# Kernel tuning notes

Measured on AMD Instinct MI355X. Metric: run time of the kernel, lower is better.

## Reference

```python
import jax, jax.numpy as jnp
import numpy as np

D_MODEL = 1024
NUM_HEADS = 16
HEAD_DIM = D_MODEL // NUM_HEADS


def setup_inputs() -> dict:
    key = jax.random.key(0)
    k_x, k_wqkv, k_bqkv, k_wout, k_bout = jax.random.split(key, 5)
    B, S = 2, 2048
    x = jax.random.normal(k_x, (B, S, D_MODEL), dtype=jnp.float32)
    # haiku Linear: y = x @ W + b, W shape [in, out]
    init_scale = 1.0 / np.sqrt(D_MODEL)
    W_qkv = jax.random.normal(k_wqkv, (D_MODEL, 3 * D_MODEL), dtype=jnp.float32) * init_scale
    b_qkv = jnp.zeros((3 * D_MODEL,), dtype=jnp.float32)
    W_out = jax.random.normal(k_wout, (D_MODEL, D_MODEL), dtype=jnp.float32) * init_scale
    b_out = jnp.zeros((D_MODEL,), dtype=jnp.float32)
    return {"x": x, "W_qkv": W_qkv, "b_qkv": b_qkv, "W_out": W_out, "b_out": b_out}


def reference(x, W_qkv, b_qkv, W_out, b_out):
    B, S, _ = x.shape
    qkv = x @ W_qkv + b_qkv                      # [B, S, 3*D]
    q, k, v = jnp.split(qkv, 3, axis=-1)         # each [B, S, D]
    # [B, S, D] -> [B, H, S, Hd]
    def heads(t):
        return t.reshape(B, S, NUM_HEADS, HEAD_DIM).transpose(0, 2, 1, 3)
    q, k, v = heads(q), heads(k), heads(v)
    scale = jnp.sqrt(jnp.float32(HEAD_DIM)).astype(x.dtype)
    attn = jnp.einsum('bhqd,bhkd->bhqk', q, k) / scale   # [B, H, S, S]
    attn = jax.nn.softmax(attn, axis=-1)
    out = jnp.einsum('bhqk,bhkd->bhqd', attn, v)          # [B, H, S, Hd]
    out = out.transpose(0, 2, 1, 3).reshape(B, S, D_MODEL)
    return out @ W_out + b_out
```

## Files before the change

kernel.cpp:

```cpp
#include <hip/hip_runtime.h>
#include <stdint.h>


#define BATCH 2
#define SEQ 2048
#define DM 1024
#define NH 16
#define HD 64
#define M_TOT 4096
#define QSCALE 0.18033688011112042f

typedef __bf16 bf16x8 __attribute__((ext_vector_type(8)));
typedef __bf16 bf16x4 __attribute__((ext_vector_type(4)));
typedef float  f32x4  __attribute__((ext_vector_type(4)));

__device__ __forceinline__ void gld_lds16(const void* g, void* l) {
    __builtin_amdgcn_global_load_lds(
        (const __attribute__((address_space(1))) uint32_t*)g,
        (__attribute__((address_space(3))) uint32_t*)l, 16, 0, 0);
}

__launch_bounds__(256)
__global__ void prep_kernel(const float* __restrict__ x,
                            const float* __restrict__ Wqkv,
                            const float* __restrict__ Wout,
                            __bf16* __restrict__ xs,
                            __bf16* __restrict__ wqt,
                            __bf16* __restrict__ wot)
{
    __shared__ float T[64][69];
    const int tid = threadIdx.x;
    const int blk = blockIdx.x;

    if (blk < 4096) {
        const int i  = blk * 256 + tid;
        const int m  = i >> 8;
        const int c4 = (i & 255) * 4;
        float4 v = *reinterpret_cast<const float4*>(&x[(size_t)m * DM + c4]);
        float a[4] = {v.x, v.y, v.z, v.w};
        bf16x4 hi, lo;
        #pragma unroll
        for (int j = 0; j < 4; ++j) {
            __bf16 h = (__bf16)a[j];
            hi[j] = h;
            lo[j] = (__bf16)(a[j] - (float)h);
        }
        *reinterpret_cast<bf16x4*>(&xs[(size_t)m * (2*DM) + c4]) = hi;
        *reinterpret_cast<bf16x4*>(&xs[(size_t)m * (2*DM) + DM + c4]) = lo;
        return;
    }

    const int bb = (blk < 4864) ? blk - 4096 : blk - 4864;
    const float* W = (blk < 4864) ? Wqkv : Wout;
    __bf16* Wt     = (blk < 4864) ? wqt  : wot;
    const int N    = (blk < 4864) ? 3 * DM : DM;
    const int k0 = (bb & 15) * 64, n0 = (bb >> 4) * 64;

    {
        const int kr = tid >> 4, c4 = (tid & 15) * 4;
        #pragma unroll
        for (int i = 0; i < 4; ++i) {
            float4 v = *reinterpret_cast<const float4*>(
                &W[(size_t)(k0 + kr + 16 * i) * N + n0 + c4]);
            *reinterpret_cast<float4*>(&T[kr + 16 * i][c4]) = v;
        }
    }
    __syncthreads();
    {
        const int n = tid >> 2, kc = (tid & 3) * 16;
        __bf16 hi[16], lo[16];
        #pragma unroll
        for (int j = 0; j < 16; ++j) {
            float v = T[kc + j][n];
            __bf16 h = (__bf16)v;
            hi[j] = h;
            lo[j] = (__bf16)(v - (float)h);
        }
        const size_t ro = (size_t)(n0 + n) * (2*DM) + k0 + kc;
        *reinterpret_cast<bf16x8*>(&Wt[ro])          = *reinterpret_cast<bf16x8*>(&hi[0]);
        *reinterpret_cast<bf16x8*>(&Wt[ro + 8])      = *reinterpret_cast<bf16x8*>(&hi[8]);
        *reinterpret_cast<bf16x8*>(&Wt[ro + DM])     = *reinterpret_cast<bf16x8*>(&lo[0]);
        *reinterpret_cast<bf16x8*>(&Wt[ro + DM + 8]) = *reinterpret_cast<bf16x8*>(&lo[8]);
    }
}

__launch_bounds__(512, 2)
__global__ void gemm_qkv_kernel(const __bf16* __restrict__ A,
                                const __bf16* __restrict__ Bt,
                                const float* __restrict__ bias,
                                __bf16* __restrict__ qs,
                                __bf16* __restrict__ khi_g,
                                __bf16* __restrict__ klo_g,
                                __bf16* __restrict__ vt_g)
{
    __shared__ __align__(16) __bf16 pool[65536];

    const int tid  = threadIdx.x;
    const int w    = tid >> 6;
    const int lane = tid & 63;
    const int n16  = lane & 15;
    const int quad = lane >> 4;

    const int wg = (blockIdx.x & 7) * 24 + (blockIdx.x >> 3);
    const int bm = (wg & 15) * 256;
    const int bn = (wg >> 4) * 256;

    const int wm = (w >> 2) * 128;
    const int wn = (w & 3) * 64;

    const int r0 = tid >> 3;
    const int c0 = ((tid & 7) ^ (r0 & 7));

    auto stage = [&](int p, int kcol, int nbuf) {
        __bf16* dst = pool + nbuf * 32768 + p * 8192;
        const __bf16* gsrc = (p < 2)
            ? A  + (size_t)(bm + p * 128) * (2*DM) + kcol
            : Bt + (size_t)(bn + (p - 2) * 128) * (2*DM) + kcol;
        gld_lds16(gsrc + (size_t)r0 * (2*DM) + c0 * 8,        dst + (size_t)tid * 8);
        gld_lds16(gsrc + (size_t)(r0 + 64) * (2*DM) + c0 * 8, dst + (size_t)(512 + tid) * 8);
    };

    const int rowA = (wm + n16) * 64;
    const int rowB = (wn + n16) * 64;
    const int sx0 = ((quad)     ^ (n16 & 7)) << 3;
    const int sx1 = ((4 + quad) ^ (n16 & 7)) << 3;

    f32x4 acc[8][4] = {};
    bf16x8 af[4][2], bf0[2][2], bf1[2][2];

    stage(0, 0, 0); stage(1, 0, 0); stage(2, 0, 0); stage(3, 0, 0);

    #pragma unroll 2
    for (int t = 0; t < 48; ++t) {
        const int buf = t & 1;
        const __bf16* bufA = pool + buf * 32768;
        const __bf16* bufB = bufA + 16384;
        const int nbuf = buf ^ 1;
        const bool pre = (t < 47);
        const int tt = t + 1;
        const int a_k = (tt < 16) ? tt * 64 : tt * 64 - DM;
        const int b_k = (tt < 32) ? tt * 64 : tt * 64 - 2 * DM;

        if (pre) {
            stage(0, a_k, nbuf);
            asm volatile("s_waitcnt vmcnt(2)" ::: "memory");
        } else {
            asm volatile("s_waitcnt vmcnt(0)" ::: "memory");
        }
        __builtin_amdgcn_s_barrier();
        __builtin_amdgcn_sched_barrier(0);
        #pragma unroll
        for (int i = 0; i < 4; ++i) {
            af[i][0] = *reinterpret_cast<const bf16x8*>(bufA + rowA + i * 1024 + sx0);
            af[i][1] = *reinterpret_cast<const bf16x8*>(bufA + rowA + i * 1024 + sx1);
        }
        #pragma unroll
        for (int j = 0; j < 2; ++j) {
            bf0[j][0] = *reinterpret_cast<const bf16x8*>(bufB + rowB + j * 1024 + sx0);
            bf0[j][1] = *reinterpret_cast<const bf16x8*>(bufB + rowB + j * 1024 + sx1);
        }
        asm volatile("s_waitcnt lgkmcnt(0)" ::: "memory");
        __builtin_amdgcn_sched_barrier(0);
        __builtin_amdgcn_s_setprio(1);
        #pragma unroll
        for (int i = 0; i < 4; ++i)
            #pragma unroll
            for (int j = 0; j < 2; ++j) {
                acc[i][j] = __builtin_amdgcn_mfma_f32_16x16x32_bf16(af[i][0], bf0[j][0], acc[i][j], 0, 0, 0);
                acc[i][j] = __builtin_amdgcn_mfma_f32_16x16x32_bf16(af[i][1], bf0[j][1], acc[i][j], 0, 0, 0);
            }
        __builtin_amdgcn_s_setprio(0);

        #pragma unroll
        for (int j = 0; j < 2; ++j) {
            bf1[j][0] = *reinterpret_cast<const bf16x8*>(bufB + rowB + (2 + j) * 1024 + sx0);
            bf1[j][1] = *reinterpret_cast<const bf16x8*>(bufB + rowB + (2 + j) * 1024 + sx1);
        }
        if (pre) stage(1, a_k, nbuf);
        __builtin_amdgcn_s_barrier();
        __builtin_amdgcn_sched_barrier(0);
        asm volatile("s_waitcnt lgkmcnt(0)" ::: "memory");
        __builtin_amdgcn_sched_barrier(0);
        __builtin_amdgcn_s_setprio(1);
        #pragma unroll
        for (int i = 0; i < 4; ++i)
            #pragma unroll
            for (int j = 0; j < 2; ++j) {
                acc[i][2 + j] = __builtin_amdgcn_mfma_f32_16x16x32_bf16(af[i][0], bf1[j][0], acc[i][2 + j], 0, 0, 0);
                acc[i][2 + j] = __builtin_amdgcn_mfma_f32_16x16x32_bf16(af[i][1], bf1[j][1], acc[i][2 + j], 0, 0, 0);
            }
        __builtin_amdgcn_s_setprio(0);

        #pragma unroll
        for (int i = 0; i < 4; ++i) {
            af[i][0] = *reinterpret_cast<const bf16x8*>(bufA + rowA + (4 + i) * 1024 + sx0);
            af[i][1] = *reinterpret_cast<const bf16x8*>(bufA + rowA + (4 + i) * 1024 + sx1);
        }
        if (pre) stage(2, b_k, nbuf);
        __builtin_amdgcn_s_barrier();
        __builtin_amdgcn_sched_barrier(0);
        asm volatile("s_waitcnt lgkmcnt(0)" ::: "memory");
        __builtin_amdgcn_sched_barrier(0);
        __builtin_amdgcn_s_setprio(1);
        #pragma unroll
        for (int i = 0; i < 4; ++i)
            #pragma unroll
            for (int j = 0; j < 2; ++j) {
                acc[4 + i][j] = __builtin_amdgcn_mfma_f32_16x16x32_bf16(af[i][0], bf0[j][0], acc[4 + i][j], 0, 0, 0);
                acc[4 + i][j] = __builtin_amdgcn_mfma_f32_16x16x32_bf16(af[i][1], bf0[j][1], acc[4 + i][j], 0, 0, 0);
            }
        __builtin_amdgcn_s_setprio(0);

        if (pre) stage(3, b_k, nbuf);
        __builtin_amdgcn_s_barrier();
        __builtin_amdgcn_sched_barrier(0);
        __builtin_amdgcn_s_setprio(1);
        #pragma unroll
        for (int i = 0; i < 4; ++i)
            #pragma unroll
            for (int j = 0; j < 2; ++j) {
                acc[4 + i][2 + j] = __builtin_amdgcn_mfma_f32_16x16x32_bf16(af[i][0], bf1[j][0], acc[4 + i][2 + j], 0, 0, 0);
                acc[4 + i][2 + j] = __builtin_amdgcn_mfma_f32_16x16x32_bf16(af[i][1], bf1[j][1], acc[4 + i][2 + j], 0, 0, 0);
            }
        __builtin_amdgcn_s_setprio(0);
    }

    __syncthreads();

    const int colb = bn + wn;
    const int part = colb >> 10;
    const int hh   = (colb & 1023) >> 6;

    float bv[4];
    #pragma unroll
    for (int j = 0; j < 4; ++j) bv[j] = bias[colb + j * 16 + n16];

    __bf16* scrH = pool + w * 4608;
    __bf16* scrL = scrH + 2304;
    const int lr = lane & 31, hc = lane >> 5;

    #pragma unroll
    for (int mi = 0; mi < 2; ++mi) {
        const int brow = bm + wm + mi * 64;
        const int b    = brow >> 11;
        const int s0   = brow & 2047;
        const int bh   = b * NH + hh;
        const int kt   = s0 >> 6;
        const size_t tb = ((size_t)bh * 32 + kt) * 4096;

        #pragma unroll
        for (int p = 0; p < 2; ++p) {
            if (part == 2) {
                #pragma unroll
                for (int jj = 0; jj < 2; ++jj) {
                    const int j = 2 * p + jj;
                    #pragma unroll
                    for (int i = 0; i < 4; ++i) {
                        bf16x4 v4;
                        #pragma unroll
                        for (int r = 0; r < 4; ++r)
                            v4[r] = (__bf16)(acc[4 * mi + i][j][r] + bv[j]);
                        *reinterpret_cast<bf16x4*>(
                            &scrH[(jj * 16 + n16) * 72 + i * 16 + quad * 4]) = v4;
                    }
                }
            } else {
                #pragma unroll
                for (int ii = 0; ii < 2; ++ii) {
                    const int i = 2 * p + ii;
                    #pragma unroll
                    for (int j = 0; j < 4; ++j) {
                        #pragma unroll
                        for (int r = 0; r < 4; ++r) {
                            float val = acc[4 * mi + i][j][r] + bv[j];
                            if (part == 0) val *= QSCALE;
                            __bf16 h = (__bf16)val;
                            const int so = (ii * 16 + quad * 4 + r) * 72 + j * 16 + n16;
                            scrH[so] = h;
                            scrL[so] = (__bf16)(val - (float)h);
                        }
                    }
                }
            }
            __syncthreads();

            if (part == 0) {
                const size_t qbase = ((size_t)bh * SEQ + s0 + 32 * p + lr) * 128;
                #pragma unroll
                for (int t = 0; t < 4; ++t) {
                    const int ch = hc * 4 + t;
                    *reinterpret_cast<bf16x8*>(&qs[qbase + ch * 8]) =
                        *reinterpret_cast<const bf16x8*>(&scrH[lr * 72 + ch * 8]);
                    *reinterpret_cast<bf16x8*>(&qs[qbase + 64 + ch * 8]) =
                        *reinterpret_cast<const bf16x8*>(&scrL[lr * 72 + ch * 8]);
                }
            } else if (part == 1) {
                const int kr = 32 * p + lr;
                #pragma unroll
                for (int t = 0; t < 4; ++t) {
                    const int ch = hc * 4 + t;
                    const int src = (ch ^ (lr & 7)) * 8;
                    *reinterpret_cast<bf16x8*>(&khi_g[tb + kr * 64 + ch * 8]) =
                        *reinterpret_cast<const bf16x8*>(&scrH[lr * 72 + src]);
                    *reinterpret_cast<bf16x8*>(&klo_g[tb + kr * 64 + ch * 8]) =
                        *reinterpret_cast<const bf16x8*>(&scrL[lr * 72 + src]);
                }
            } else {
                const int d = 32 * p + lr;
                #pragma unroll
                for (int t = 0; t < 4; ++t) {
                    const int ch = hc * 4 + t;
                    const int src = (ch ^ (lr & 7)) * 8;
                    *reinterpret_cast<bf16x8*>(&vt_g[tb + d * 64 + ch * 8]) =
                        *reinterpret_cast<const bf16x8*>(&scrH[lr * 72 + src]);
                }
            }
            __syncthreads();
        }
    }
}

__launch_bounds__(256)
__global__ void gemm_out_kernel(const __bf16* __restrict__ A,
                                const __bf16* __restrict__ Bt,
                                const float* __restrict__ bias,
                                float* __restrict__ out)
{
    __shared__ __align__(16) __bf16 AsH[128 * 32];
    __shared__ __align__(16) __bf16 AsL[128 * 32];
    __shared__ __align__(16) __bf16 BsH[64 * 32];
    __shared__ __align__(16) __bf16 BsL[64 * 32];

    const int tid  = threadIdx.x;
    const int w    = tid >> 6;
    const int lane = tid & 63;
    const int n16  = lane & 15;
    const int quad = lane >> 4;
    const int bm = blockIdx.x * 128, bn = blockIdx.y * 64;
    const int wm = (w & 1) * 64,     wn = (w >> 1) * 32;

    const int srow = tid >> 2, sc = (tid & 3) * 8;
    const __bf16* Ar = A  + (size_t)(bm + srow) * (2*DM) + sc;
    const __bf16* Br = Bt + (size_t)(bn + srow) * (2*DM) + sc;

    f32x4 acc[4][2] = {};

    for (int k0 = 0; k0 < DM; k0 += 32) {
        __syncthreads();
        gld_lds16(Ar + k0,                         &AsH[(size_t)tid * 8]);
        gld_lds16(Ar + k0 + (size_t)64*2*DM,       &AsH[(size_t)(256 + tid) * 8]);
        gld_lds16(Ar + DM + k0,                    &AsL[(size_t)tid * 8]);
        gld_lds16(Ar + DM + k0 + (size_t)64*2*DM,  &AsL[(size_t)(256 + tid) * 8]);
        gld_lds16(Br + k0,                         &BsH[(size_t)tid * 8]);
        gld_lds16(Br + DM + k0,                    &BsL[(size_t)tid * 8]);
        __syncthreads();

        bf16x8 afh[4], afl[4], bfh[2], bfl[2];
        #pragma unroll
        for (int i = 0; i < 4; ++i) {
            const int ro = (wm + i*16 + n16) * 32 + quad * 8;
            afh[i] = *reinterpret_cast<const bf16x8*>(&AsH[ro]);
            afl[i] = *reinterpret_cast<const bf16x8*>(&AsL[ro]);
        }
        #pragma unroll
        for (int j = 0; j < 2; ++j) {
            const int ro = (wn + j*16 + n16) * 32 + quad * 8;
            bfh[j] = *reinterpret_cast<const bf16x8*>(&BsH[ro]);
            bfl[j] = *reinterpret_cast<const bf16x8*>(&BsL[ro]);
        }
        #pragma unroll
        for (int i = 0; i < 4; ++i)
            #pragma unroll
            for (int j = 0; j < 2; ++j) {
                acc[i][j] = __builtin_amdgcn_mfma_f32_16x16x32_bf16(afh[i], bfh[j], acc[i][j], 0, 0, 0);
                acc[i][j] = __builtin_amdgcn_mfma_f32_16x16x32_bf16(afh[i], bfl[j], acc[i][j], 0, 0, 0);
                acc[i][j] = __builtin_amdgcn_mfma_f32_16x16x32_bf16(afl[i], bfh[j], acc[i][j], 0, 0, 0);
            }
    }

    #pragma unroll
    for (int j = 0; j < 2; ++j) {
        const int col = bn + wn + j * 16 + n16;
        const float bvv = bias[col];
        #pragma unroll
        for (int i = 0; i < 4; ++i) {
            const int row0 = bm + wm + i * 16 + quad * 4;
            #pragma unroll
            for (int r = 0; r < 4; ++r)
                out[(size_t)(row0 + r) * DM + col] = acc[i][j][r] + bvv;
        }
    }
}

__launch_bounds__(256, 2)
__global__ void flash_attn_v5_kernel(const __bf16* __restrict__ qs,
                                     const __bf16* __restrict__ khi_g,
                                     const __bf16* __restrict__ klo_g,
                                     const __bf16* __restrict__ vt_g,
                                     __bf16* __restrict__ ctx2)
{
    __shared__ __align__(16) __bf16 Khi[2][4096];
    __shared__ __align__(16) __bf16 Klo[2][4096];
    __shared__ __align__(16) __bf16 Vt [2][4096];
    __shared__ __align__(16) __bf16 Ps [8192];

    const int tid  = threadIdx.x;
    const int w    = tid >> 6;
    const int lane = tid & 63;
    const int n16  = lane & 15;
    const int quad = lane >> 4;
    const int bid  = blockIdx.x;
    const int bh = (bid & 7) * 4 + (bid >> 7);
    const int qt = (bid >> 3) & 15;

    bf16x8 qh[2][2], ql[2][2];
    #pragma unroll
    for (int qg = 0; qg < 2; ++qg) {
        const size_t qrow =
            ((size_t)bh * SEQ + qt * 128 + w * 32 + qg * 16 + n16) * 128;
        #pragma unroll
        for (int s2 = 0; s2 < 2; ++s2) {
            qh[qg][s2] = *reinterpret_cast<const bf16x8*>(&qs[qrow + s2 * 32 + quad * 8]);
            ql[qg][s2] = *reinterpret_cast<const bf16x8*>(&qs[qrow + 64 + s2 * 32 + quad * 8]);
        }
    }

    f32x4 o[2][4] = {};
    float l_lane[2] = {};

    for (int kt2 = 0; kt2 < 16; ++kt2) {
        __syncthreads();
        {
            const int buf = w >> 1;
            const size_t tb = ((size_t)bh * 32 + kt2 * 2 + buf) * 4096;
            #pragma unroll
            for (int t = 0; t < 12; ++t) {
                const int rem = (w & 1) * 12 + t;
                const int arr = rem >> 3, sub = rem & 7;
                const int eo = sub * 512 + lane * 8;
                const __bf16* g = (arr == 0 ? khi_g : arr == 1 ? klo_g : vt_g) + tb + eo;
                __bf16* l = (arr == 0 ? Khi[buf] : arr == 1 ? Klo[buf] : Vt[buf]) + eo;
                gld_lds16(g, l);
            }
        }
        __syncthreads();

        #pragma unroll
        for (int hf = 0; hf < 2; ++hf) {
            const __bf16* KhiB = Khi[hf];
            const __bf16* KloB = Klo[hf];
            const __bf16* VtB  = Vt[hf];

            #pragma unroll
            for (int kg = 0; kg < 4; ++kg) {
                const int r = kg * 16 + n16;
                const int o0 = r * 64 + ((quad ^ (r & 7)) << 3);
                const int o1 = r * 64 + (((4 + quad) ^ (r & 7)) << 3);
                bf16x8 kh0 = *reinterpret_cast<const bf16x8*>(&KhiB[o0]);
                bf16x8 kl0 = *reinterpret_cast<const bf16x8*>(&KloB[o0]);
                bf16x8 kh1 = *reinterpret_cast<const bf16x8*>(&KhiB[o1]);
                bf16x8 kl1 = *reinterpret_cast<const bf16x8*>(&KloB[o1]);
                #pragma unroll
                for (int qg = 0; qg < 2; ++qg) {
                    f32x4 sa = {}, sb = {};
                    sa = __builtin_amdgcn_mfma_f32_16x16x32_bf16(kh0, qh[qg][0], sa, 0, 0, 0);
                    sb = __builtin_amdgcn_mfma_f32_16x16x32_bf16(kh1, qh[qg][1], sb, 0, 0, 0);
                    sa = __builtin_amdgcn_mfma_f32_16x16x32_bf16(kl0, qh[qg][0], sa, 0, 0, 0);
                    sb = __builtin_amdgcn_mfma_f32_16x16x32_bf16(kl1, qh[qg][1], sb, 0, 0, 0);
                    sa = __builtin_amdgcn_mfma_f32_16x16x32_bf16(kh0, ql[qg][0], sa, 0, 0, 0);
                    sb = __builtin_amdgcn_mfma_f32_16x16x32_bf16(kh1, ql[qg][1], sb, 0, 0, 0);
                    f32x4 st = sa + sb;

                    f32x4 pp;
                    #pragma unroll
                    for (int r2 = 0; r2 < 4; ++r2) pp[r2] = exp2f(st[r2]);
                    l_lane[qg] += (pp[0] + pp[1]) + (pp[2] + pp[3]);

                    bf16x4 p4;
                    #pragma unroll
                    for (int r2 = 0; r2 < 4; ++r2) p4[r2] = (__bf16)pp[r2];
                    const int prow = w * 32 + qg * 16 + n16;
                    const int ch2 = kg * 2 + (quad >> 1);
                    const int off = prow * 64 + ((ch2 ^ (prow & 7)) << 3) + (quad & 1) * 4;
                    *reinterpret_cast<bf16x4*>(&Ps[off]) = p4;
                }
            }

            bf16x8 pa[2][2];
            #pragma unroll
            for (int qg = 0; qg < 2; ++qg) {
                const int prow = w * 32 + qg * 16 + n16;
                #pragma unroll
                for (int s2 = 0; s2 < 2; ++s2)
                    pa[qg][s2] = *reinterpret_cast<const bf16x8*>(
                        &Ps[prow * 64 + (((s2 * 4 + quad) ^ (prow & 7)) << 3)]);
            }
            #pragma unroll
            for (int c = 0; c < 4; ++c) {
                const int vr = c * 16 + n16;
                bf16x8 vb0 = *reinterpret_cast<const bf16x8*>(
                    &VtB[vr * 64 + ((quad ^ (vr & 7)) << 3)]);
                bf16x8 vb1 = *reinterpret_cast<const bf16x8*>(
                    &VtB[vr * 64 + (((4 + quad) ^ (vr & 7)) << 3)]);
                #pragma unroll
                for (int qg = 0; qg < 2; ++qg) {
                    o[qg][c] = __builtin_amdgcn_mfma_f32_16x16x32_bf16(pa[qg][0], vb0, o[qg][c], 0, 0, 0);
                    o[qg][c] = __builtin_amdgcn_mfma_f32_16x16x32_bf16(pa[qg][1], vb1, o[qg][c], 0, 0, 0);
                }
            }
        }
    }

    #pragma unroll
    for (int qg = 0; qg < 2; ++qg) {
        l_lane[qg] += __shfl_xor(l_lane[qg], 16, 64);
        l_lane[qg] += __shfl_xor(l_lane[qg], 32, 64);
    }

    const int b = bh >> 4, hh = bh & 15;
    #pragma unroll
    for (int qg = 0; qg < 2; ++qg) {
        #pragma unroll
        for (int r2 = 0; r2 < 4; ++r2) {
            const float l = __shfl(l_lane[qg], (quad << 4) + quad * 4 + r2, 64);
            const float linv = 1.0f / l;
            const int srow = qt * 128 + w * 32 + qg * 16 + quad * 4 + r2;
            const size_t rowoff = (size_t)(b * SEQ + srow) * (2*DM);
            #pragma unroll
            for (int c = 0; c < 4; ++c) {
                const int col = hh * HD + c * 16 + n16;
                float v = o[qg][c][r2] * linv;
                __bf16 h = (__bf16)v;
                ctx2[rowoff + col] = h;
                ctx2[rowoff + DM + col] = (__bf16)(v - (float)h);
            }
        }
    }
}

extern "C" void kernel_launch(void* const* d_in, const int* in_sizes, int n_in,
                              void* d_out, int out_size, void* d_ws, size_t ws_size,
                              hipStream_t stream)
{
    const float* x    = (const float*)d_in[0];
    const float* Wqkv = (const float*)d_in[1];
    const float* bqkv = (const float*)d_in[2];
    const float* Wout = (const float*)d_in[3];
    const float* bout = (const float*)d_in[4];
    float* out = (float*)d_out;

    char* ws = (char*)d_ws;
    __bf16* xs   = (__bf16*)(ws);
    __bf16* ctx2 = xs;
    __bf16* wqt  = (__bf16*)(ws + (size_t)16 * 1024 * 1024);
    __bf16* wot  = (__bf16*)(ws + (size_t)28 * 1024 * 1024);
    __bf16* qsb  = (__bf16*)(ws + (size_t)32 * 1024 * 1024);
    __bf16* khi  = (__bf16*)(ws + (size_t)48 * 1024 * 1024);
    __bf16* klo  = (__bf16*)(ws + (size_t)56 * 1024 * 1024);
    __bf16* vt   = (__bf16*)(ws + (size_t)64 * 1024 * 1024);

    prep_kernel<<<dim3(5120), 256, 0, stream>>>(x, Wqkv, Wout, xs, wqt, wot);
    gemm_qkv_kernel<<<dim3(192), 512, 0, stream>>>(
        xs, wqt, bqkv, qsb, khi, klo, vt);
    flash_attn_v5_kernel<<<dim3(512), 256, 0, stream>>>(qsb, khi, klo, vt, ctx2);
    gemm_out_kernel<<<dim3(M_TOT / 128, DM / 64), 256, 0, stream>>>(
        ctx2, wot, bout, out);
}
```

Baseline: 284.0 us.

## Double-buffer attention K/V tiles and issue all GEMM prefetches up front

In the QKV GEMM main loop, all four global-to-LDS stage copies for the next k-tile are now issued at the start of the iteration instead of being spread between the MFMA phases. The wait becomes vmcnt(8) so only the current tile's loads must land. In the attention kernel, the old loop loaded two 64-key half tiles into LDS with two block-wide syncs and then computed on them. It is replaced by a 32-step double-buffered pipeline: the next tile is prefetched asynchronously while the current one is computed, with a trailing barrier guarding buffer reuse. The aim is to hide global load latency behind MFMA work, at the cost of more in-flight loads and a few extra barriers.

```diff
diff --git a/kernel.cpp b/kernel.cpp
--- a/kernel.cpp
+++ b/kernel.cpp
@@ -143,7 +143,10 @@
 
         if (pre) {
             stage(0, a_k, nbuf);
-            asm volatile("s_waitcnt vmcnt(2)" ::: "memory");
+            stage(1, a_k, nbuf);
+            stage(2, b_k, nbuf);
+            stage(3, b_k, nbuf);
+            asm volatile("s_waitcnt vmcnt(8)" ::: "memory");
         } else {
             asm volatile("s_waitcnt vmcnt(0)" ::: "memory");
         }
@@ -176,7 +179,6 @@
             bf1[j][0] = *reinterpret_cast<const bf16x8*>(bufB + rowB + (2 + j) * 1024 + sx0);
             bf1[j][1] = *reinterpret_cast<const bf16x8*>(bufB + rowB + (2 + j) * 1024 + sx1);
         }
-        if (pre) stage(1, a_k, nbuf);
         __builtin_amdgcn_s_barrier();
         __builtin_amdgcn_sched_barrier(0);
         asm volatile("s_waitcnt lgkmcnt(0)" ::: "memory");
@@ -196,7 +198,6 @@
             af[i][0] = *reinterpret_cast<const bf16x8*>(bufA + rowA + (4 + i) * 1024 + sx0);
             af[i][1] = *reinterpret_cast<const bf16x8*>(bufA + rowA + (4 + i) * 1024 + sx1);
         }
-        if (pre) stage(2, b_k, nbuf);
         __builtin_amdgcn_s_barrier();
         __builtin_amdgcn_sched_barrier(0);
         asm volatile("s_waitcnt lgkmcnt(0)" ::: "memory");
@@ -211,7 +212,6 @@
             }
         __builtin_amdgcn_s_setprio(0);
 
-        if (pre) stage(3, b_k, nbuf);
         __builtin_amdgcn_s_barrier();
         __builtin_amdgcn_sched_barrier(0);
         __builtin_amdgcn_s_setprio(1);
@@ -428,87 +428,97 @@
     f32x4 o[2][4] = {};
     float l_lane[2] = {};
 
-    for (int kt2 = 0; kt2 < 16; ++kt2) {
-        __syncthreads();
-        {
-            const int buf = w >> 1;
-            const size_t tb = ((size_t)bh * 32 + kt2 * 2 + buf) * 4096;
-            #pragma unroll
-            for (int t = 0; t < 12; ++t) {
-                const int rem = (w & 1) * 12 + t;
-                const int arr = rem >> 3, sub = rem & 7;
-                const int eo = sub * 512 + lane * 8;
-                const __bf16* g = (arr == 0 ? khi_g : arr == 1 ? klo_g : vt_g) + tb + eo;
-                __bf16* l = (arr == 0 ? Khi[buf] : arr == 1 ? Klo[buf] : Vt[buf]) + eo;
-                gld_lds16(g, l);
-            }
-        }
-        __syncthreads();
-
-        #pragma unroll
-        for (int hf = 0; hf < 2; ++hf) {
-            const __bf16* KhiB = Khi[hf];
-            const __bf16* KloB = Klo[hf];
-            const __bf16* VtB  = Vt[hf];
-
-            #pragma unroll
-            for (int kg = 0; kg < 4; ++kg) {
-                const int r = kg * 16 + n16;
-                const int o0 = r * 64 + ((quad ^ (r & 7)) << 3);
-                const int o1 = r * 64 + (((4 + quad) ^ (r & 7)) << 3);
-                bf16x8 kh0 = *reinterpret_cast<const bf16x8*>(&KhiB[o0]);
-                bf16x8 kl0 = *reinterpret_cast<const bf16x8*>(&KloB[o0]);
-                bf16x8 kh1 = *reinterpret_cast<const bf16x8*>(&KhiB[o1]);
-                bf16x8 kl1 = *reinterpret_cast<const bf16x8*>(&KloB[o1]);
-                #pragma unroll
-                for (int qg = 0; qg < 2; ++qg) {
-                    f32x4 sa = {}, sb = {};
-                    sa = __builtin_amdgcn_mfma_f32_16x16x32_bf16(kh0, qh[qg][0], sa, 0, 0, 0);
-                    sb = __builtin_amdgcn_mfma_f32_16x16x32_bf16(kh1, qh[qg][1], sb, 0, 0, 0);
-                    sa = __builtin_amdgcn_mfma_f32_16x16x32_bf16(kl0, qh[qg][0], sa, 0, 0, 0);
-                    sb = __builtin_amdgcn_mfma_f32_16x16x32_bf16(kl1, qh[qg][1], sb, 0, 0, 0);
-                    sa = __builtin_amdgcn_mfma_f32_16x16x32_bf16(kh0, ql[qg][0], sa, 0, 0, 0);
-                    sb = __builtin_amdgcn_mfma_f32_16x16x32_bf16(kh1, ql[qg][1], sb, 0, 0, 0);
-                    f32x4 st = sa + sb;
-
-                    f32x4 pp;
-                    #pragma unroll
-                    for (int r2 = 0; r2 < 4; ++r2) pp[r2] = exp2f(st[r2]);
-                    l_lane[qg] += (pp[0] + pp[1]) + (pp[2] + pp[3]);
-
-                    bf16x4 p4;
-                    #pragma unroll
-                    for (int r2 = 0; r2 < 4; ++r2) p4[r2] = (__bf16)pp[r2];
-                    const int prow = w * 32 + qg * 16 + n16;
-                    const int ch2 = kg * 2 + (quad >> 1);
-                    const int off = prow * 64 + ((ch2 ^ (prow & 7)) << 3) + (quad & 1) * 4;
-                    *reinterpret_cast<bf16x4*>(&Ps[off]) = p4;
-                }
-            }
-
-            bf16x8 pa[2][2];
+    auto stage_tile = [&](int kt, int b) {
+        const size_t tb = ((size_t)bh * 32 + kt) * 4096;
+        #pragma unroll
+        for (int t = 0; t < 6; ++t) {
+            const int c = w * 6 + t;
+            const int arr = c >> 3, sub = c & 7;
+            const int eo = sub * 512 + lane * 8;
+            const __bf16* g = (arr == 0 ? khi_g : arr == 1 ? klo_g : vt_g) + tb + eo;
+            __bf16* l = (arr == 0 ? Khi[b] : arr == 1 ? Klo[b] : Vt[b]) + eo;
+            gld_lds16(g, l);
+        }
+    };
+
+    stage_tile(0, 0);
+
+    #pragma unroll 2
+    for (int kt = 0; kt < 32; ++kt) {
+        const int cur = kt & 1;
+        if (kt < 31) {
+            stage_tile(kt + 1, cur ^ 1);
+            asm volatile("s_waitcnt vmcnt(6)" ::: "memory");
+        } else {
+            asm volatile("s_waitcnt vmcnt(0)" ::: "memory");
+        }
+        __builtin_amdgcn_s_barrier();
+        __builtin_amdgcn_sched_barrier(0);
+
+        const __bf16* KhiB = Khi[cur];
+        const __bf16* KloB = Klo[cur];
+        const __bf16* VtB  = Vt[cur];
+
+        #pragma unroll
+        for (int kg = 0; kg < 4; ++kg) {
+            const int r = kg * 16 + n16;
+            const int o0 = r * 64 + ((quad ^ (r & 7)) << 3);
+            const int o1 = r * 64 + (((4 + quad) ^ (r & 7)) << 3);
+            bf16x8 kh0 = *reinterpret_cast<const bf16x8*>(&KhiB[o0]);
+            bf16x8 kl0 = *reinterpret_cast<const bf16x8*>(&KloB[o0]);
+            bf16x8 kh1 = *reinterpret_cast<const bf16x8*>(&KhiB[o1]);
+            bf16x8 kl1 = *reinterpret_cast<const bf16x8*>(&KloB[o1]);
             #pragma unroll
             for (int qg = 0; qg < 2; ++qg) {
+                f32x4 sa = {}, sb = {};
+                sa = __builtin_amdgcn_mfma_f32_16x16x32_bf16(kh0, qh[qg][0], sa, 0, 0, 0);
+                sb = __builtin_amdgcn_mfma_f32_16x16x32_bf16(kh1, qh[qg][1], sb, 0, 0, 0);
+                sa = __builtin_amdgcn_mfma_f32_16x16x32_bf16(kl0, qh[qg][0], sa, 0, 0, 0);
+                sb = __builtin_amdgcn_mfma_f32_16x16x32_bf16(kl1, qh[qg][1], sb, 0, 0, 0);
+                sa = __builtin_amdgcn_mfma_f32_16x16x32_bf16(kh0, ql[qg][0], sa, 0, 0, 0);
+                sb = __builtin_amdgcn_mfma_f32_16x16x32_bf16(kh1, ql[qg][1], sb, 0, 0, 0);
+                f32x4 st = sa + sb;
+
+                f32x4 pp;
+                #pragma unroll
+                for (int r2 = 0; r2 < 4; ++r2) pp[r2] = exp2f(st[r2]);
+                l_lane[qg] += (pp[0] + pp[1]) + (pp[2] + pp[3]);
+
+                bf16x4 p4;
+                #pragma unroll
+                for (int r2 = 0; r2 < 4; ++r2) p4[r2] = (__bf16)pp[r2];
                 const int prow = w * 32 + qg * 16 + n16;
-                #pragma unroll
-                for (int s2 = 0; s2 < 2; ++s2)
-                    pa[qg][s2] = *reinterpret_cast<const bf16x8*>(
-                        &Ps[prow * 64 + (((s2 * 4 + quad) ^ (prow & 7)) << 3)]);
-            }
-            #pragma unroll
-            for (int c = 0; c < 4; ++c) {
-                const int vr = c * 16 + n16;
-                bf16x8 vb0 = *reinterpret_cast<const bf16x8*>(
-                    &VtB[vr * 64 + ((quad ^ (vr & 7)) << 3)]);
-                bf16x8 vb1 = *reinterpret_cast<const bf16x8*>(
-                    &VtB[vr * 64 + (((4 + quad) ^ (vr & 7)) << 3)]);
-                #pragma unroll
-                for (int qg = 0; qg < 2; ++qg) {
-                    o[qg][c] = __builtin_amdgcn_mfma_f32_16x16x32_bf16(pa[qg][0], vb0, o[qg][c], 0, 0, 0);
-                    o[qg][c] = __builtin_amdgcn_mfma_f32_16x16x32_bf16(pa[qg][1], vb1, o[qg][c], 0, 0, 0);
-                }
-            }
-        }
+                const int ch2 = kg * 2 + (quad >> 1);
+                const int off = prow * 64 + ((ch2 ^ (prow & 7)) << 3) + (quad & 1) * 4;
+                *reinterpret_cast<bf16x4*>(&Ps[off]) = p4;
+            }
+        }
+
+        bf16x8 pa[2][2];
+        #pragma unroll
+        for (int qg = 0; qg < 2; ++qg) {
+            const int prow = w * 32 + qg * 16 + n16;
+            #pragma unroll
+            for (int s2 = 0; s2 < 2; ++s2)
+                pa[qg][s2] = *reinterpret_cast<const bf16x8*>(
+                    &Ps[prow * 64 + (((s2 * 4 + quad) ^ (prow & 7)) << 3)]);
+        }
+        #pragma unroll
+        for (int c = 0; c < 4; ++c) {
+            const int vr = c * 16 + n16;
+            bf16x8 vb0 = *reinterpret_cast<const bf16x8*>(
+                &VtB[vr * 64 + ((quad ^ (vr & 7)) << 3)]);
+            bf16x8 vb1 = *reinterpret_cast<const bf16x8*>(
+                &VtB[vr * 64 + (((4 + quad) ^ (vr & 7)) << 3)]);
+            #pragma unroll
+            for (int qg = 0; qg < 2; ++qg) {
+                o[qg][c] = __builtin_amdgcn_mfma_f32_16x16x32_bf16(pa[qg][0], vb0, o[qg][c], 0, 0, 0);
+                o[qg][c] = __builtin_amdgcn_mfma_f32_16x16x32_bf16(pa[qg][1], vb1, o[qg][c], 0, 0, 0);
+            }
+        }
+
+        __builtin_amdgcn_s_barrier();
+        __builtin_amdgcn_sched_barrier(0);
     }
 
     #pragma unroll
```

After: 352.4 us. 1.24x slower.

## Split attention work across 8 waves with 16 query rows each

Applied to the files above, without the earlier changes.

The flash attention block grows from 256 to 512 threads, so each wave handles 16 query rows instead of 32 and the K/V tile loads are spread over 8 waves. This roughly halves the per-wave register footprint and gives more waves to hide latency. The cost is that each wave now reuses every K and V fragment read from LDS for only one query group, so LDS read traffic per MFMA doubles, and block-wide synchronisation spans more waves.

```diff
diff --git a/kernel.cpp b/kernel.cpp
--- a/kernel.cpp
+++ b/kernel.cpp
@@ -392,8 +392,8 @@
     }
 }
 
-__launch_bounds__(256, 2)
-__global__ void flash_attn_v5_kernel(const __bf16* __restrict__ qs,
+__launch_bounds__(512, 2)
+__global__ void flash_attn_v6_kernel(const __bf16* __restrict__ qs,
                                      const __bf16* __restrict__ khi_g,
                                      const __bf16* __restrict__ klo_g,
                                      const __bf16* __restrict__ vt_g,
@@ -413,29 +413,28 @@
     const int bh = (bid & 7) * 4 + (bid >> 7);
     const int qt = (bid >> 3) & 15;
 
-    bf16x8 qh[2][2], ql[2][2];
-    #pragma unroll
-    for (int qg = 0; qg < 2; ++qg) {
+    bf16x8 qh[2], ql[2];
+    {
         const size_t qrow =
-            ((size_t)bh * SEQ + qt * 128 + w * 32 + qg * 16 + n16) * 128;
+            ((size_t)bh * SEQ + qt * 128 + w * 16 + n16) * 128;
         #pragma unroll
         for (int s2 = 0; s2 < 2; ++s2) {
-            qh[qg][s2] = *reinterpret_cast<const bf16x8*>(&qs[qrow + s2 * 32 + quad * 8]);
-            ql[qg][s2] = *reinterpret_cast<const bf16x8*>(&qs[qrow + 64 + s2 * 32 + quad * 8]);
-        }
-    }
-
-    f32x4 o[2][4] = {};
-    float l_lane[2] = {};
+            qh[s2] = *reinterpret_cast<const bf16x8*>(&qs[qrow + s2 * 32 + quad * 8]);
+            ql[s2] = *reinterpret_cast<const bf16x8*>(&qs[qrow + 64 + s2 * 32 + quad * 8]);
+        }
+    }
+
+    f32x4 o[4] = {};
+    float l_lane = 0.f;
 
     for (int kt2 = 0; kt2 < 16; ++kt2) {
         __syncthreads();
         {
-            const int buf = w >> 1;
+            const int buf = w >> 2;
             const size_t tb = ((size_t)bh * 32 + kt2 * 2 + buf) * 4096;
             #pragma unroll
-            for (int t = 0; t < 12; ++t) {
-                const int rem = (w & 1) * 12 + t;
+            for (int t = 0; t < 6; ++t) {
+                const int rem = (w & 3) * 6 + t;
                 const int arr = rem >> 3, sub = rem & 7;
                 const int eo = sub * 512 + lane * 8;
                 const __bf16* g = (arr == 0 ? khi_g : arr == 1 ? klo_g : vt_g) + tb + eo;
@@ -460,39 +459,36 @@
                 bf16x8 kl0 = *reinterpret_cast<const bf16x8*>(&KloB[o0]);
                 bf16x8 kh1 = *reinterpret_cast<const bf16x8*>(&KhiB[o1]);
                 bf16x8 kl1 = *reinterpret_cast<const bf16x8*>(&KloB[o1]);
-                #pragma unroll
-                for (int qg = 0; qg < 2; ++qg) {
-                    f32x4 sa = {}, sb = {};
-                    sa = __builtin_amdgcn_mfma_f32_16x16x32_bf16(kh0, qh[qg][0], sa, 0, 0, 0);
-                    sb = __builtin_amdgcn_mfma_f32_16x16x32_bf16(kh1, qh[qg][1], sb, 0, 0, 0);
-                    sa = __builtin_amdgcn_mfma_f32_16x16x32_bf16(kl0, qh[qg][0], sa, 0, 0, 0);
-                    sb = __builtin_amdgcn_mfma_f32_16x16x32_bf16(kl1, qh[qg][1], sb, 0, 0, 0);
-                    sa = __builtin_amdgcn_mfma_f32_16x16x32_bf16(kh0, ql[qg][0], sa, 0, 0, 0);
-                    sb = __builtin_amdgcn_mfma_f32_16x16x32_bf16(kh1, ql[qg][1], sb, 0, 0, 0);
-                    f32x4 st = sa + sb;
-
-                    f32x4 pp;
-                    #pragma unroll
-                    for (int r2 = 0; r2 < 4; ++r2) pp[r2] = exp2f(st[r2]);
-                    l_lane[qg] += (pp[0] + pp[1]) + (pp[2] + pp[3]);
-
-                    bf16x4 p4;
-                    #pragma unroll
-                    for (int r2 = 0; r2 < 4; ++r2) p4[r2] = (__bf16)pp[r2];
-                    const int prow = w * 32 + qg * 16 + n16;
-                    const int ch2 = kg * 2 + (quad >> 1);
-                    const int off = prow * 64 + ((ch2 ^ (prow & 7)) << 3) + (quad & 1) * 4;
-                    *reinterpret_cast<bf16x4*>(&Ps[off]) = p4;
-                }
-            }
-
-            bf16x8 pa[2][2];
-            #pragma unroll
-            for (int qg = 0; qg < 2; ++qg) {
-                const int prow = w * 32 + qg * 16 + n16;
+
+                f32x4 sa = {}, sb = {};
+                sa = __builtin_amdgcn_mfma_f32_16x16x32_bf16(kh0, qh[0], sa, 0, 0, 0);
+                sb = __builtin_amdgcn_mfma_f32_16x16x32_bf16(kh1, qh[1], sb, 0, 0, 0);
+                sa = __builtin_amdgcn_mfma_f32_16x16x32_bf16(kl0, qh[0], sa, 0, 0, 0);
+                sb = __builtin_amdgcn_mfma_f32_16x16x32_bf16(kl1, qh[1], sb, 0, 0, 0);
+                sa = __builtin_amdgcn_mfma_f32_16x16x32_bf16(kh0, ql[0], sa, 0, 0, 0);
+                sb = __builtin_amdgcn_mfma_f32_16x16x32_bf16(kh1, ql[1], sb, 0, 0, 0);
+                f32x4 st = sa + sb;
+
+                f32x4 pp;
+                #pragma unroll
+                for (int r2 = 0; r2 < 4; ++r2) pp[r2] = exp2f(st[r2]);
+                l_lane += (pp[0] + pp[1]) + (pp[2] + pp[3]);
+
+                bf16x4 p4;
+                #pragma unroll
+                for (int r2 = 0; r2 < 4; ++r2) p4[r2] = (__bf16)pp[r2];
+                const int prow = w * 16 + n16;
+                const int ch2 = kg * 2 + (quad >> 1);
+                const int off = prow * 64 + ((ch2 ^ (prow & 7)) << 3) + (quad & 1) * 4;
+                *reinterpret_cast<bf16x4*>(&Ps[off]) = p4;
+            }
+
+            bf16x8 pa[2];
+            {
+                const int prow = w * 16 + n16;
                 #pragma unroll
                 for (int s2 = 0; s2 < 2; ++s2)
-                    pa[qg][s2] = *reinterpret_cast<const bf16x8*>(
+                    pa[s2] = *reinterpret_cast<const bf16x8*>(
                         &Ps[prow * 64 + (((s2 * 4 + quad) ^ (prow & 7)) << 3)]);
             }
             #pragma unroll
@@ -502,38 +498,29 @@
                     &VtB[vr * 64 + ((quad ^ (vr & 7)) << 3)]);
                 bf16x8 vb1 = *reinterpret_cast<const bf16x8*>(
                     &VtB[vr * 64 + (((4 + quad) ^ (vr & 7)) << 3)]);
-                #pragma unroll
-                for (int qg = 0; qg < 2; ++qg) {
-                    o[qg][c] = __builtin_amdgcn_mfma_f32_16x16x32_bf16(pa[qg][0], vb0, o[qg][c], 0, 0, 0);
-                    o[qg][c] = __builtin_amdgcn_mfma_f32_16x16x32_bf16(pa[qg][1], vb1, o[qg][c], 0, 0, 0);
-                }
-            }
-        }
-    }
-
-    #pragma unroll
-    for (int qg = 0; qg < 2; ++qg) {
-        l_lane[qg] += __shfl_xor(l_lane[qg], 16, 64);
-        l_lane[qg] += __shfl_xor(l_lane[qg], 32, 64);
-    }
+                o[c] = __builtin_amdgcn_mfma_f32_16x16x32_bf16(pa[0], vb0, o[c], 0, 0, 0);
+                o[c] = __builtin_amdgcn_mfma_f32_16x16x32_bf16(pa[1], vb1, o[c], 0, 0, 0);
+            }
+        }
+    }
+
+    l_lane += __shfl_xor(l_lane, 16, 64);
+    l_lane += __shfl_xor(l_lane, 32, 64);
 
     const int b = bh >> 4, hh = bh & 15;
     #pragma unroll
-    for (int qg = 0; qg < 2; ++qg) {
-        #pragma unroll
-        for (int r2 = 0; r2 < 4; ++r2) {
-            const float l = __shfl(l_lane[qg], (quad << 4) + quad * 4 + r2, 64);
-            const float linv = 1.0f / l;
-            const int srow = qt * 128 + w * 32 + qg * 16 + quad * 4 + r2;
-            const size_t rowoff = (size_t)(b * SEQ + srow) * (2*DM);
-            #pragma unroll
-            for (int c = 0; c < 4; ++c) {
-                const int col = hh * HD + c * 16 + n16;
-                float v = o[qg][c][r2] * linv;
-                __bf16 h = (__bf16)v;
-                ctx2[rowoff + col] = h;
-                ctx2[rowoff + DM + col] = (__bf16)(v - (float)h);
-            }
+    for (int r2 = 0; r2 < 4; ++r2) {
+        const float l = __shfl(l_lane, (quad << 4) + quad * 4 + r2, 64);
+        const float linv = 1.0f / l;
+        const int srow = qt * 128 + w * 16 + quad * 4 + r2;
+        const size_t rowoff = (size_t)(b * SEQ + srow) * (2*DM);
+        #pragma unroll
+        for (int c = 0; c < 4; ++c) {
+            const int col = hh * HD + c * 16 + n16;
+            float v = o[c][r2] * linv;
+            __bf16 h = (__bf16)v;
+            ctx2[rowoff + col] = h;
+            ctx2[rowoff + DM + col] = (__bf16)(v - (float)h);
         }
     }
 }
@@ -562,7 +549,7 @@
     prep_kernel<<<dim3(5120), 256, 0, stream>>>(x, Wqkv, Wout, xs, wqt, wot);
     gemm_qkv_kernel<<<dim3(192), 512, 0, stream>>>(
         xs, wqt, bqkv, qsb, khi, klo, vt);
-    flash_attn_v5_kernel<<<dim3(512), 256, 0, stream>>>(qsb, khi, klo, vt, ctx2);
+    flash_attn_v6_kernel<<<dim3(512), 512, 0, stream>>>(qsb, khi, klo, vt, ctx2);
     gemm_out_kernel<<<dim3(M_TOT / 128, DM / 64), 256, 0, stream>>>(
         ctx2, wot, bout, out);
 }
```

After: 284.2 us (median of 2 runs). Within noise of the previous version (+0.1%).
